# Kernel tuning notes

Measured on AMD Instinct MI355X. Metric: run time of the kernel, lower is better.

Reference implementation:

```python
import jax, jax.numpy as jnp
import numpy as np

N = 10000
E = 320000
C = 16


def gcn_conv(x, edge_index, W, b, num_nodes):
    # PyG GCNConv: h = X W, then symmetric-normalized aggregation with self-loops, then + b
    h = x @ W  # [N, F_out]
    loop = jnp.arange(num_nodes, dtype=edge_index.dtype)
    src = jnp.concatenate([edge_index[0], loop])
    dst = jnp.concatenate([edge_index[1], loop])
    ones = jnp.ones(src.shape[0], dtype=h.dtype)
    deg = jax.ops.segment_sum(ones, dst, num_segments=num_nodes)  # in-degree incl. self-loop
    dinv = jnp.where(deg > 0, jax.lax.rsqrt(deg), 0.0)
    norm = dinv[src] * dinv[dst]  # [E+N]
    msg = h[src] * norm[:, None]  # gather + scale
    out = jax.ops.segment_sum(msg, dst, num_segments=num_nodes)  # scatter-add
    return out + b


def setup_inputs() -> dict:
    key = jax.random.key(0)
    ks = jax.random.split(key, 8)
    x = jax.random.normal(ks[0], (N, N), dtype=jnp.float32)
    edge_index = jax.random.randint(ks[1], (2, E), 0, N, dtype=jnp.int64)
    W1 = jax.random.normal(ks[2], (N, 64), dtype=jnp.float32) * (1.0 / np.sqrt(N))
    b1 = jnp.zeros((64,), dtype=jnp.float32)
    W2 = jax.random.normal(ks[3], (64, 64), dtype=jnp.float32) * (1.0 / 8.0)
    b2 = jnp.zeros((64,), dtype=jnp.float32)
    W3 = jax.random.normal(ks[4], (64, C), dtype=jnp.float32) * (1.0 / 8.0)
    b3 = jnp.zeros((C,), dtype=jnp.float32)
    return {"x": x, "edge_index": edge_index, "W1": W1, "b1": b1,
            "W2": W2, "b2": b2, "W3": W3, "b3": b3}


def reference(x, edge_index, W1, b1, W2, b2, W3, b3):
    h = jax.nn.relu(gcn_conv(x, edge_index, W1, b1, N))
    h = jax.nn.relu(gcn_conv(h, edge_index, W2, b2, N))
    h = gcn_conv(h, edge_index, W3, b3, N)
    return jax.nn.softmax(h, axis=1)
```

## Files before the change

### kernel.cpp

```cpp
#include <hip/hip_runtime.h>

#define N_NODES 10000
#define E_EDGES 320000
#define KP 10016

typedef float f32x4 __attribute__((ext_vector_type(4)));
typedef __bf16 bf16x8 __attribute__((ext_vector_type(8)));

union frag_u { int4 i; bf16x8 b; };

static __device__ __forceinline__ ushort f2bf(float f) {
    unsigned u = __float_as_uint(f);
    unsigned r = (u + 0x7fffu + ((u >> 16) & 1u)) >> 16;
    return (ushort)r;
}
static __device__ __forceinline__ float bf2f(ushort h) {
    return __uint_as_float(((unsigned)h) << 16);
}

static __device__ __forceinline__ void split2(float f0, float f1,
                                              unsigned& hi, unsigned& lo) {
    unsigned u0 = __float_as_uint(f0), u1 = __float_as_uint(f1);
    hi = __builtin_amdgcn_perm(u1, u0, 0x07060302u);
    float h0 = __uint_as_float(u0 & 0xFFFF0000u);
    float h1 = __uint_as_float(u1 & 0xFFFF0000u);
    float l0 = f0 - h0, l1 = f1 - h1;
    lo = __builtin_amdgcn_perm(__float_as_uint(l1), __float_as_uint(l0), 0x07060302u);
}

static __device__ __forceinline__ void load16_to_lds(const float* gp, void* lp) {
    __builtin_amdgcn_global_load_lds(
        (__attribute__((address_space(1))) void*)(gp),
        (__attribute__((address_space(3))) void*)(lp), 16, 0, 0);
}


__global__ void k_hist(const int* __restrict__ dst, int* __restrict__ deg) {
    int e = blockIdx.x * blockDim.x + threadIdx.x;
    if (e < E_EDGES) atomicAdd(&deg[dst[e]], 1);
}

__global__ void k_dinv(const int* __restrict__ deg, float* __restrict__ dinv) {
    int i = blockIdx.x * blockDim.x + threadIdx.x;
    if (i < N_NODES) dinv[i] = rsqrtf(1.0f + (float)deg[i]);
}

__global__ void k_scan(const int* __restrict__ deg, int* __restrict__ roff) {
    __shared__ int sums[256];
    __shared__ int offs[256];
    const int CH = 40;
    int t = threadIdx.x;
    int base = t * CH;
    int s = 0;
    for (int i = 0; i < CH; i++) {
        int idx = base + i;
        if (idx < N_NODES) s += deg[idx];
    }
    sums[t] = s;
    __syncthreads();
    if (t == 0) {
        int r = 0;
        for (int i = 0; i < 256; i++) { offs[i] = r; r += sums[i]; }
    }
    __syncthreads();
    int r = offs[t];
    for (int i = 0; i < CH; i++) {
        int idx = base + i;
        if (idx < N_NODES) { roff[idx] = r; r += deg[idx]; }
    }
    if (t == 255) roff[N_NODES] = E_EDGES;
}

__global__ void k_scatter(const int* __restrict__ src, const int* __restrict__ dst,
                          const int* __restrict__ roff, int* __restrict__ cursor,
                          const float* __restrict__ dinv,
                          int* __restrict__ csrc, float* __restrict__ cw) {
    int e = blockIdx.x * blockDim.x + threadIdx.x;
    if (e >= E_EDGES) return;
    int s = src[e], d = dst[e];
    int slot = roff[d] + atomicAdd(&cursor[d], 1);
    csrc[slot] = s;
    cw[slot] = dinv[s] * dinv[d];
}


__global__ void k_wsplit(const float* __restrict__ W1, ushort* __restrict__ Whi,
                         ushort* __restrict__ Wlo) {
    int k = blockIdx.x * 256 + threadIdx.x;
    int n = blockIdx.y;
    if (k >= KP) return;
    ushort h = 0, l = 0;
    if (k < N_NODES) {
        float f = W1[(long)k * 64 + n];
        h = f2bf(f);
        l = f2bf(f - bf2f(h));
    }
    Whi[(long)n * KP + k] = h;
    Wlo[(long)n * KP + k] = l;
}


#define G1_BM 128
#define G1_CHUNK 640
#define G1_NCHUNK 16

__global__ __launch_bounds__(256) void k_gemm1_mfma(
        const float* __restrict__ x, const ushort* __restrict__ Whi,
        const ushort* __restrict__ Wlo, float* __restrict__ out) {
    __shared__ float As32[G1_BM][32];
    __shared__ ushort Bs[2][64][40];

    int tid = threadIdx.x;
    int lane = tid & 63, wv = tid >> 6;
    int quad = lane >> 4, lm = lane & 15;
    int m0 = blockIdx.x * G1_BM;
    int ks = blockIdx.y * G1_CHUNK;
    int ke = min(ks + G1_CHUNK, KP);

    int rown = lane >> 3;
    int sp = (lane & 7) ^ rown;
    long abase[4];
#pragma unroll
    for (int i = 0; i < 4; i++) {
        int row = (wv * 4 + i) * 8 + rown;
        int gm = min(m0 + row, N_NODES - 1);
        abase[i] = (long)gm * N_NODES + sp * 4;
    }
    const long FLAT_MAX = (long)N_NODES * N_NODES - 4;

    int bn = tid >> 2, bp = (tid & 3) * 8;
    const ushort* whip = Whi + (long)bn * KP + bp;
    const ushort* wlop = Wlo + (long)bn * KP + bp;

    f32x4 acc[2][4] = {};

    for (int k0 = ks; k0 < ke; k0 += 32) {
#pragma unroll
        for (int i = 0; i < 4; i++) {
            long flat = abase[i] + k0;
            if (flat > FLAT_MAX) flat = FLAT_MAX;
            load16_to_lds(x + flat, &As32[(wv * 4 + i) * 8][0]);
        }
        float4 vh = *(const float4*)(whip + k0);
        float4 vl = *(const float4*)(wlop + k0);
        *(float4*)&Bs[0][bn][bp] = vh;
        *(float4*)&Bs[1][bn][bp] = vl;
        __syncthreads();

        frag_u ah[2], al[2];
#pragma unroll
        for (int r = 0; r < 2; r++) {
            int row = wv * 32 + r * 16 + lm;
            int r7 = row & 7;
            int s0 = (quad * 2) ^ r7;
            int s1 = (quad * 2 + 1) ^ r7;
            float4 fa = *(const float4*)&As32[row][s0 * 4];
            float4 fb = *(const float4*)&As32[row][s1 * 4];
            unsigned h0, l0, h1, l1, h2, l2, h3, l3;
            split2(fa.x, fa.y, h0, l0);
            split2(fa.z, fa.w, h1, l1);
            split2(fb.x, fb.y, h2, l2);
            split2(fb.z, fb.w, h3, l3);
            ah[r].i = make_int4((int)h0, (int)h1, (int)h2, (int)h3);
            al[r].i = make_int4((int)l0, (int)l1, (int)l2, (int)l3);
        }
        frag_u bh[4], bl[4];
#pragma unroll
        for (int c = 0; c < 4; c++) {
            int n = c * 16 + lm;
            bh[c].b = *(const bf16x8*)&Bs[0][n][quad * 8];
            bl[c].b = *(const bf16x8*)&Bs[1][n][quad * 8];
        }
#pragma unroll
        for (int r = 0; r < 2; r++)
#pragma unroll
            for (int c = 0; c < 4; c++) {
                acc[r][c] = __builtin_amdgcn_mfma_f32_16x16x32_bf16(al[r].b, bh[c].b, acc[r][c], 0, 0, 0);
                acc[r][c] = __builtin_amdgcn_mfma_f32_16x16x32_bf16(ah[r].b, bl[c].b, acc[r][c], 0, 0, 0);
                acc[r][c] = __builtin_amdgcn_mfma_f32_16x16x32_bf16(ah[r].b, bh[c].b, acc[r][c], 0, 0, 0);
            }
        __syncthreads();
    }

#pragma unroll
    for (int r = 0; r < 2; r++)
#pragma unroll
        for (int c = 0; c < 4; c++) {
            int row0 = m0 + wv * 32 + r * 16 + quad * 4;
            int cn = c * 16 + lm;
#pragma unroll
            for (int i = 0; i < 4; i++) {
                int gm = row0 + i;
                if (gm < N_NODES) atomicAdd(&out[gm * 64 + cn], acc[r][c][i]);
            }
        }
}


__global__ void k_gemm64(const float* __restrict__ in, const float* __restrict__ W,
                         float* __restrict__ out) {
    __shared__ float Ws[64 * 64];
    __shared__ float Ain[4][64];
    int tid = threadIdx.x;
    int tx = tid & 63, ty = tid >> 6;
    for (int f = tid; f < 1024; f += 256)
        *(float4*)&Ws[f * 4] = *(const float4*)&W[f * 4];
    int gm = blockIdx.x * 4 + ty;
    Ain[ty][tx] = in[gm * 64 + tx];
    __syncthreads();
    float acc = 0.f;
#pragma unroll
    for (int k = 0; k < 64; k++) acc = fmaf(Ain[ty][k], Ws[k * 64 + tx], acc);
    out[gm * 64 + tx] = acc;
}

__global__ void k_gemm16(const float* __restrict__ in, const float* __restrict__ W,
                         float* __restrict__ out) {
    __shared__ float Ws[64 * 16];
    __shared__ float Ain[16][64];
    int tid = threadIdx.x;
    int tx = tid & 15, ty = tid >> 4;
    *(float4*)&Ws[tid * 4] = *(const float4*)&W[tid * 4];
    {
        int r = tid >> 4, kq = tid & 15;
        *(float4*)&Ain[r][kq * 4] =
            *(const float4*)(in + (long)(blockIdx.x * 16 + r) * 64 + kq * 4);
    }
    __syncthreads();
    float acc = 0.f;
#pragma unroll
    for (int k = 0; k < 64; k++) acc = fmaf(Ain[ty][k], Ws[k * 16 + tx], acc);
    out[(blockIdx.x * 16 + ty) * 16 + tx] = acc;
}


__global__ void k_agg64(const float* __restrict__ h, const float* __restrict__ bias,
                        const int* __restrict__ roff, const int* __restrict__ csrc,
                        const float* __restrict__ cw, const float* __restrict__ dinv,
                        float* __restrict__ out, int do_relu) {
    int n = blockIdx.x * 4 + (threadIdx.x >> 6);
    int c = threadIdx.x & 63;
    float di = dinv[n];
    float acc = di * di * h[n * 64 + c];
    int e0 = roff[n], e1 = roff[n + 1];
    int e = e0;
    for (; e + 3 < e1; e += 4) {
        int s0 = csrc[e], s1 = csrc[e + 1], s2 = csrc[e + 2], s3 = csrc[e + 3];
        float w0 = cw[e], w1 = cw[e + 1], w2 = cw[e + 2], w3 = cw[e + 3];
        float v0 = h[s0 * 64 + c], v1 = h[s1 * 64 + c];
        float v2 = h[s2 * 64 + c], v3 = h[s3 * 64 + c];
        acc = fmaf(w0, v0, acc);
        acc = fmaf(w1, v1, acc);
        acc = fmaf(w2, v2, acc);
        acc = fmaf(w3, v3, acc);
    }
    for (; e < e1; e++)
        acc = fmaf(cw[e], h[csrc[e] * 64 + c], acc);
    acc += bias[c];
    if (do_relu) acc = fmaxf(acc, 0.f);
    out[n * 64 + c] = acc;
}

__global__ void k_agg16_softmax(const float* __restrict__ h, const float* __restrict__ b3,
                                const int* __restrict__ roff, const int* __restrict__ csrc,
                                const float* __restrict__ cw, const float* __restrict__ dinv,
                                float* __restrict__ out) {
    int lane = threadIdx.x & 63;
    int n = blockIdx.x * 4 + (threadIdx.x >> 6);
    int c = lane & 15, g = lane >> 4;
    float di = dinv[n];
    float acc = (g == 0) ? di * di * h[n * 16 + c] : 0.f;
    int e0 = roff[n], e1 = roff[n + 1];
    for (int e = e0 + g; e < e1; e += 4)
        acc = fmaf(cw[e], h[csrc[e] * 16 + c], acc);
    acc += __shfl_xor(acc, 16);
    acc += __shfl_xor(acc, 32);
    float logit = acc + b3[c];
    float m = logit;
    m = fmaxf(m, __shfl_xor(m, 1));
    m = fmaxf(m, __shfl_xor(m, 2));
    m = fmaxf(m, __shfl_xor(m, 4));
    m = fmaxf(m, __shfl_xor(m, 8));
    float ex = expf(logit - m);
    float s = ex;
    s += __shfl_xor(s, 1);
    s += __shfl_xor(s, 2);
    s += __shfl_xor(s, 4);
    s += __shfl_xor(s, 8);
    if (g == 0) out[n * 16 + c] = ex / s;
}


extern "C" void kernel_launch(void* const* d_in, const int* in_sizes, int n_in,
                              void* d_out, int out_size, void* d_ws, size_t ws_size,
                              hipStream_t stream) {
    (void)in_sizes; (void)n_in; (void)out_size; (void)ws_size;
    const float* x  = (const float*)d_in[0];
    const int*   ei = (const int*)d_in[1];
    const float* W1 = (const float*)d_in[2];
    const float* b1 = (const float*)d_in[3];
    const float* W2 = (const float*)d_in[4];
    const float* b2 = (const float*)d_in[5];
    const float* W3 = (const float*)d_in[6];
    const float* b3 = (const float*)d_in[7];
    float* out = (float*)d_out;
    const int* esrc = ei;
    const int* edst = ei + E_EDGES;

    char* p = (char*)d_ws;
    size_t off = 0;
    auto alloc = [&](size_t b) -> void* {
        void* r = p + off;
        off += (b + 255) & ~(size_t)255;
        return r;
    };
    int*    deg    = (int*)alloc(N_NODES * 4);
    int*    cursor = (int*)alloc(N_NODES * 4);
    int*    roff   = (int*)alloc((N_NODES + 1) * 4);
    float*  dinv   = (float*)alloc(N_NODES * 4);
    int*    csrc   = (int*)alloc(E_EDGES * 4);
    float*  cw     = (float*)alloc(E_EDGES * 4);
    float*  bufA   = (float*)alloc(N_NODES * 64 * 4);
    float*  bufB   = (float*)alloc(N_NODES * 64 * 4);
    float*  bufC   = (float*)alloc(N_NODES * 16 * 4);
    ushort* Whi    = (ushort*)alloc((size_t)64 * KP * 2);
    ushort* Wlo    = (ushort*)alloc((size_t)64 * KP * 2);

    hipMemsetAsync(deg, 0, N_NODES * 4, stream);
    hipMemsetAsync(cursor, 0, N_NODES * 4, stream);
    hipMemsetAsync(bufA, 0, N_NODES * 64 * 4, stream);

    k_hist<<<(E_EDGES + 255) / 256, 256, 0, stream>>>(edst, deg);
    k_dinv<<<(N_NODES + 255) / 256, 256, 0, stream>>>(deg, dinv);
    k_scan<<<1, 256, 0, stream>>>(deg, roff);
    k_scatter<<<(E_EDGES + 255) / 256, 256, 0, stream>>>(esrc, edst, roff, cursor, dinv,
                                                         csrc, cw);
    k_wsplit<<<dim3((KP + 255) / 256, 64), 256, 0, stream>>>(W1, Whi, Wlo);

    k_gemm1_mfma<<<dim3((N_NODES + G1_BM - 1) / G1_BM, G1_NCHUNK), 256, 0, stream>>>(
        x, Whi, Wlo, bufA);
    k_agg64<<<N_NODES / 4, 256, 0, stream>>>(bufA, b1, roff, csrc, cw, dinv, bufB, 1);
    k_gemm64<<<N_NODES / 4, 256, 0, stream>>>(bufB, W2, bufA);
    k_agg64<<<N_NODES / 4, 256, 0, stream>>>(bufA, b2, roff, csrc, cw, dinv, bufB, 1);
    k_gemm16<<<N_NODES / 16, 256, 0, stream>>>(bufB, W3, bufC);
    k_agg16_softmax<<<N_NODES / 4, 256, 0, stream>>>(bufC, b3, roff, csrc, cw, dinv, out);
}
```

Measured before the change: 689.2 us.

## Fuse small GCN layer kernels and merge preprocessing launches

Layers 2 and 3 now aggregate first and then apply the dense weight inside the same kernel, using the identity A(HW) = (AH)W. This removes the separate small GEMM kernels and the intermediate buffers. The histogram and weight-split kernels are merged into one launch, dinv is computed inside the scan, and the three memsets become one contiguous memset. Layer 3 now aggregates 64-wide rows instead of 16-wide ones, which raises gather traffic for that layer in exchange for fewer launches.

After: 687.0 us. Within noise of the previous version (-0.3%).

```diff
diff --git a/kernel.cpp b/kernel.cpp
--- a/kernel.cpp
+++ b/kernel.cpp
@@ -35,17 +35,38 @@
 }
 
 
-__global__ void k_hist(const int* __restrict__ dst, int* __restrict__ deg) {
-    int e = blockIdx.x * blockDim.x + threadIdx.x;
-    if (e < E_EDGES) atomicAdd(&deg[dst[e]], 1);
-}
-
-__global__ void k_dinv(const int* __restrict__ deg, float* __restrict__ dinv) {
-    int i = blockIdx.x * blockDim.x + threadIdx.x;
-    if (i < N_NODES) dinv[i] = rsqrtf(1.0f + (float)deg[i]);
-}
-
-__global__ void k_scan(const int* __restrict__ deg, int* __restrict__ roff) {
+#define HIST_BLOCKS (E_EDGES / 256)
+#define WSPLIT_KB   ((KP + 255) / 256)
+#define WSPLIT_BLOCKS (WSPLIT_KB * 64)
+
+__global__ void k_hist_wsplit(const int* __restrict__ dst, int* __restrict__ deg,
+                              const float* __restrict__ W1, ushort* __restrict__ Whi,
+                              ushort* __restrict__ Wlo) {
+    int bid = blockIdx.x;
+    int tid = threadIdx.x;
+    if (bid < HIST_BLOCKS) {
+        int e = bid * 256 + tid;
+        atomicAdd(&deg[dst[e]], 1);
+    } else {
+        int q = bid - HIST_BLOCKS;
+        int n = q / WSPLIT_KB;
+        int kb = q % WSPLIT_KB;
+        int k = kb * 256 + tid;
+        if (k >= KP) return;
+        ushort h = 0, l = 0;
+        if (k < N_NODES) {
+            float f = W1[(long)k * 64 + n];
+            h = f2bf(f);
+            l = f2bf(f - bf2f(h));
+        }
+        Whi[(long)n * KP + k] = h;
+        Wlo[(long)n * KP + k] = l;
+    }
+}
+
+
+__global__ void k_scan(const int* __restrict__ deg, int* __restrict__ roff,
+                       float* __restrict__ dinv) {
     __shared__ int sums[256];
     __shared__ int offs[256];
     const int CH = 40;
@@ -54,7 +75,11 @@
     int s = 0;
     for (int i = 0; i < CH; i++) {
         int idx = base + i;
-        if (idx < N_NODES) s += deg[idx];
+        if (idx < N_NODES) {
+            int d = deg[idx];
+            s += d;
+            dinv[idx] = rsqrtf(1.0f + (float)d);
+        }
     }
     sums[t] = s;
     __syncthreads();
@@ -81,22 +106,6 @@
     int slot = roff[d] + atomicAdd(&cursor[d], 1);
     csrc[slot] = s;
     cw[slot] = dinv[s] * dinv[d];
-}
-
-
-__global__ void k_wsplit(const float* __restrict__ W1, ushort* __restrict__ Whi,
-                         ushort* __restrict__ Wlo) {
-    int k = blockIdx.x * 256 + threadIdx.x;
-    int n = blockIdx.y;
-    if (k >= KP) return;
-    ushort h = 0, l = 0;
-    if (k < N_NODES) {
-        float f = W1[(long)k * 64 + n];
-        h = f2bf(f);
-        l = f2bf(f - bf2f(h));
-    }
-    Whi[(long)n * KP + k] = h;
-    Wlo[(long)n * KP + k] = l;
 }
 
 
@@ -194,43 +203,6 @@
                 if (gm < N_NODES) atomicAdd(&out[gm * 64 + cn], acc[r][c][i]);
             }
         }
-}
-
-
-__global__ void k_gemm64(const float* __restrict__ in, const float* __restrict__ W,
-                         float* __restrict__ out) {
-    __shared__ float Ws[64 * 64];
-    __shared__ float Ain[4][64];
-    int tid = threadIdx.x;
-    int tx = tid & 63, ty = tid >> 6;
-    for (int f = tid; f < 1024; f += 256)
-        *(float4*)&Ws[f * 4] = *(const float4*)&W[f * 4];
-    int gm = blockIdx.x * 4 + ty;
-    Ain[ty][tx] = in[gm * 64 + tx];
-    __syncthreads();
-    float acc = 0.f;
-#pragma unroll
-    for (int k = 0; k < 64; k++) acc = fmaf(Ain[ty][k], Ws[k * 64 + tx], acc);
-    out[gm * 64 + tx] = acc;
-}
-
-__global__ void k_gemm16(const float* __restrict__ in, const float* __restrict__ W,
-                         float* __restrict__ out) {
-    __shared__ float Ws[64 * 16];
-    __shared__ float Ain[16][64];
-    int tid = threadIdx.x;
-    int tx = tid & 15, ty = tid >> 4;
-    *(float4*)&Ws[tid * 4] = *(const float4*)&W[tid * 4];
-    {
-        int r = tid >> 4, kq = tid & 15;
-        *(float4*)&Ain[r][kq * 4] =
-            *(const float4*)(in + (long)(blockIdx.x * 16 + r) * 64 + kq * 4);
-    }
-    __syncthreads();
-    float acc = 0.f;
-#pragma unroll
-    for (int k = 0; k < 64; k++) acc = fmaf(Ain[ty][k], Ws[k * 16 + tx], acc);
-    out[(blockIdx.x * 16 + ty) * 16 + tx] = acc;
 }
 
 
@@ -261,21 +233,94 @@
     out[n * 64 + c] = acc;
 }
 
-__global__ void k_agg16_softmax(const float* __restrict__ h, const float* __restrict__ b3,
-                                const int* __restrict__ roff, const int* __restrict__ csrc,
-                                const float* __restrict__ cw, const float* __restrict__ dinv,
-                                float* __restrict__ out) {
-    int lane = threadIdx.x & 63;
-    int n = blockIdx.x * 4 + (threadIdx.x >> 6);
-    int c = lane & 15, g = lane >> 4;
+
+__global__ __launch_bounds__(256) void k_layer2(
+        const float* __restrict__ h, const float* __restrict__ W2,
+        const float* __restrict__ b2,
+        const int* __restrict__ roff, const int* __restrict__ csrc,
+        const float* __restrict__ cw, const float* __restrict__ dinv,
+        float* __restrict__ out) {
+    __shared__ float Ws[64 * 64];
+    __shared__ float rowbuf[4][64];
+    int tid = threadIdx.x;
+    int w = tid >> 6, c = tid & 63;
+    for (int f = tid; f < 1024; f += 256)
+        *(float4*)&Ws[f * 4] = *(const float4*)&W2[f * 4];
+
+    int n = blockIdx.x * 4 + w;
     float di = dinv[n];
-    float acc = (g == 0) ? di * di * h[n * 16 + c] : 0.f;
+    float acc = di * di * h[n * 64 + c];
     int e0 = roff[n], e1 = roff[n + 1];
-    for (int e = e0 + g; e < e1; e += 4)
-        acc = fmaf(cw[e], h[csrc[e] * 16 + c], acc);
-    acc += __shfl_xor(acc, 16);
-    acc += __shfl_xor(acc, 32);
-    float logit = acc + b3[c];
+    int e = e0;
+    for (; e + 3 < e1; e += 4) {
+        int s0 = csrc[e], s1 = csrc[e + 1], s2 = csrc[e + 2], s3 = csrc[e + 3];
+        float w0 = cw[e], w1 = cw[e + 1], w2 = cw[e + 2], w3 = cw[e + 3];
+        float v0 = h[s0 * 64 + c], v1 = h[s1 * 64 + c];
+        float v2 = h[s2 * 64 + c], v3 = h[s3 * 64 + c];
+        acc = fmaf(w0, v0, acc);
+        acc = fmaf(w1, v1, acc);
+        acc = fmaf(w2, v2, acc);
+        acc = fmaf(w3, v3, acc);
+    }
+    for (; e < e1; e++)
+        acc = fmaf(cw[e], h[csrc[e] * 64 + c], acc);
+    rowbuf[w][c] = acc;
+    __syncthreads();
+
+    float o = b2[c];
+#pragma unroll
+    for (int k = 0; k < 64; k++)
+        o = fmaf(rowbuf[w][k], Ws[k * 64 + c], o);
+    o = fmaxf(o, 0.f);
+    out[n * 64 + c] = o;
+}
+
+
+__global__ __launch_bounds__(256) void k_layer3(
+        const float* __restrict__ h, const float* __restrict__ W3,
+        const float* __restrict__ b3,
+        const int* __restrict__ roff, const int* __restrict__ csrc,
+        const float* __restrict__ cw, const float* __restrict__ dinv,
+        float* __restrict__ out) {
+    __shared__ float Ws[64 * 17];
+    __shared__ float rowbuf[4][64];
+    int tid = threadIdx.x;
+    int w = tid >> 6, c = tid & 63;
+    for (int f = tid; f < 1024; f += 256) {
+        int kk = f >> 4, cc0 = f & 15;
+        Ws[kk * 17 + cc0] = W3[f];
+    }
+
+    int n = blockIdx.x * 4 + w;
+    float di = dinv[n];
+    float acc = di * di * h[n * 64 + c];
+    int e0 = roff[n], e1 = roff[n + 1];
+    int e = e0;
+    for (; e + 3 < e1; e += 4) {
+        int s0 = csrc[e], s1 = csrc[e + 1], s2 = csrc[e + 2], s3 = csrc[e + 3];
+        float w0 = cw[e], w1 = cw[e + 1], w2 = cw[e + 2], w3 = cw[e + 3];
+        float v0 = h[s0 * 64 + c], v1 = h[s1 * 64 + c];
+        float v2 = h[s2 * 64 + c], v3 = h[s3 * 64 + c];
+        acc = fmaf(w0, v0, acc);
+        acc = fmaf(w1, v1, acc);
+        acc = fmaf(w2, v2, acc);
+        acc = fmaf(w3, v3, acc);
+    }
+    for (; e < e1; e++)
+        acc = fmaf(cw[e], h[csrc[e] * 64 + c], acc);
+    rowbuf[w][c] = acc;
+    __syncthreads();
+
+    int cc = c & 15, g = c >> 4;
+    float o = 0.f;
+#pragma unroll
+    for (int i = 0; i < 16; i++) {
+        int k = g * 16 + i;
+        o = fmaf(rowbuf[w][k], Ws[k * 17 + cc], o);
+    }
+    o += __shfl_xor(o, 16);
+    o += __shfl_xor(o, 32);
+    float logit = o + b3[cc];
     float m = logit;
     m = fmaxf(m, __shfl_xor(m, 1));
     m = fmaxf(m, __shfl_xor(m, 2));
@@ -287,7 +332,7 @@
     s += __shfl_xor(s, 2);
     s += __shfl_xor(s, 4);
     s += __shfl_xor(s, 8);
-    if (g == 0) out[n * 16 + c] = ex / s;
+    if (g == 0) out[n * 16 + cc] = ex / s;
 }
 
 
@@ -316,32 +361,26 @@
     };
     int*    deg    = (int*)alloc(N_NODES * 4);
     int*    cursor = (int*)alloc(N_NODES * 4);
+    float*  bufA   = (float*)alloc(N_NODES * 64 * 4);
     int*    roff   = (int*)alloc((N_NODES + 1) * 4);
     float*  dinv   = (float*)alloc(N_NODES * 4);
     int*    csrc   = (int*)alloc(E_EDGES * 4);
     float*  cw     = (float*)alloc(E_EDGES * 4);
-    float*  bufA   = (float*)alloc(N_NODES * 64 * 4);
     float*  bufB   = (float*)alloc(N_NODES * 64 * 4);
-    float*  bufC   = (float*)alloc(N_NODES * 16 * 4);
     ushort* Whi    = (ushort*)alloc((size_t)64 * KP * 2);
     ushort* Wlo    = (ushort*)alloc((size_t)64 * KP * 2);
 
-    hipMemsetAsync(deg, 0, N_NODES * 4, stream);
-    hipMemsetAsync(cursor, 0, N_NODES * 4, stream);
-    hipMemsetAsync(bufA, 0, N_NODES * 64 * 4, stream);
-
-    k_hist<<<(E_EDGES + 255) / 256, 256, 0, stream>>>(edst, deg);
-    k_dinv<<<(N_NODES + 255) / 256, 256, 0, stream>>>(deg, dinv);
-    k_scan<<<1, 256, 0, stream>>>(deg, roff);
+    size_t zlen = (size_t)((char*)(bufA + N_NODES * 64) - (char*)deg);
+    hipMemsetAsync(deg, 0, zlen, stream);
+
+    k_hist_wsplit<<<HIST_BLOCKS + WSPLIT_BLOCKS, 256, 0, stream>>>(edst, deg, W1, Whi, Wlo);
+    k_scan<<<1, 256, 0, stream>>>(deg, roff, dinv);
     k_scatter<<<(E_EDGES + 255) / 256, 256, 0, stream>>>(esrc, edst, roff, cursor, dinv,
                                                          csrc, cw);
-    k_wsplit<<<dim3((KP + 255) / 256, 64), 256, 0, stream>>>(W1, Whi, Wlo);
 
     k_gemm1_mfma<<<dim3((N_NODES + G1_BM - 1) / G1_BM, G1_NCHUNK), 256, 0, stream>>>(
         x, Whi, Wlo, bufA);
     k_agg64<<<N_NODES / 4, 256, 0, stream>>>(bufA, b1, roff, csrc, cw, dinv, bufB, 1);
-    k_gemm64<<<N_NODES / 4, 256, 0, stream>>>(bufB, W2, bufA);
-    k_agg64<<<N_NODES / 4, 256, 0, stream>>>(bufA, b2, roff, csrc, cw, dinv, bufB, 1);
-    k_gemm16<<<N_NODES / 16, 256, 0, stream>>>(bufB, W3, bufC);
-    k_agg16_softmax<<<N_NODES / 4, 256, 0, stream>>>(bufC, b3, roff, csrc, cw, dinv, out);
-}
+    k_layer2<<<N_NODES / 4, 256, 0, stream>>>(bufB, W2, b2, roff, csrc, cw, dinv, bufA);
+    k_layer3<<<N_NODES / 4, 256, 0, stream>>>(bufA, W3, b3, roff, csrc, cw, dinv, out);
+}
```
